# Performance work log

Measured on AMD Instinct MI355X. Metric: run time of the kernel, lower is better.

The kernel has to match this reference:

```python
import jax, jax.numpy as jnp
import numpy as np

N = 100000
E = 1600000
IN_C, HID, OUT_C = 500, 256, 40
K, ALPHA = 10, 0.1
LN_EPS = 1e-5


def setup_inputs() -> dict:
    key = jax.random.key(0)
    ks = jax.random.split(key, 12)
    glorot = lambda k, i, o: jax.random.normal(k, (i, o), jnp.float32) * (1.0 / np.sqrt(i))
    return {
        "x": jax.random.normal(ks[0], (N, IN_C), jnp.float32),
        "edge_index": jax.random.randint(ks[1], (2, E), 0, N, jnp.int64),
        "W1": glorot(ks[2], IN_C, HID), "b1": jnp.zeros((HID,), jnp.float32),
        "g1": jnp.ones((HID,), jnp.float32), "be1": jnp.zeros((HID,), jnp.float32),
        "W2": glorot(ks[3], HID, HID), "b2": jnp.zeros((HID,), jnp.float32),
        "g2": jnp.ones((HID,), jnp.float32), "be2": jnp.zeros((HID,), jnp.float32),
        "W3": glorot(ks[4], HID, OUT_C), "b3": jnp.zeros((OUT_C,), jnp.float32),
    }


def _layernorm(h, g, b):
    mu = jnp.mean(h, axis=-1, keepdims=True)
    var = jnp.mean(jnp.square(h - mu), axis=-1, keepdims=True)
    return (h - mu) * jax.lax.rsqrt(var + LN_EPS) * g + b


def reference(x, edge_index, W1, b1, g1, be1, W2, b2, g2, be2, W3, b3):
    # --- MLP (eval mode: dropout inactive) ---
    h = _layernorm(jax.nn.gelu(x @ W1 + b1, approximate=False), g1, be1)
    h = _layernorm(jax.nn.gelu(h @ W2 + b2, approximate=False), g2, be2)
    h = h @ W3 + b3  # [N, OUT_C]

    # --- GCN normalization with self-loops (PyG gcn_norm) ---
    loops = jnp.arange(N, dtype=edge_index.dtype)
    row = jnp.concatenate([edge_index[0], loops])  # source
    col = jnp.concatenate([edge_index[1], loops])  # target
    deg = jax.ops.segment_sum(jnp.ones_like(col, jnp.float32), col, num_segments=N)
    dinv = jnp.where(deg > 0, jax.lax.rsqrt(deg), 0.0)
    norm = dinv[row] * dinv[col]  # [E+N]

    # --- APPNP: K steps of h <- (1-alpha) * A_hat h + alpha * h0 ---
    h0 = h
    for _ in range(K):
        msg = norm[:, None] * h[row]                       # gather + scale
        agg = jax.ops.segment_sum(msg, col, num_segments=N)  # scatter-add
        h = (1.0 - ALPHA) * agg + ALPHA * h0
    return h
```

## Files before the change

### kernel.cpp

```cpp
#include <hip/hip_runtime.h>
#include <hip/hip_bf16.h>
#include <math.h>

#define N_NODES 100000
#define N_EDGES 1600000
#define IN_C    500
#define HID     256
#define OUT_C   40
#define K_ITERS 10
#define ALPHA   0.1f
#define LN_EPS  1e-5f

#define K1PAD   512
#define K2PAD   256

#define SCAN_CHUNK 1024
#define NBLK_SCAN  ((N_NODES + SCAN_CHUNK - 1) / SCAN_CHUNK)

typedef __attribute__((ext_vector_type(8))) short bf16x8;
typedef __attribute__((ext_vector_type(4))) float f32x4;

__device__ __forceinline__ void split2(float a, short& hi, short& lo) {
    const unsigned ua = __float_as_uint(a);
    hi = (short)(ua >> 16);
    const float r = a - __uint_as_float(ua & 0xffff0000u);
    lo = (short)(__float_as_uint(r) >> 16);
}

__device__ __forceinline__ void async_load16(const void* g, void* l) {
    __builtin_amdgcn_global_load_lds(
        (const __attribute__((address_space(1))) void*)g,
        (__attribute__((address_space(3))) void*)l, 16, 0, 0);
}

__global__ void deg_count_kernel(const int* __restrict__ col, int* __restrict__ cnt, int e) {
    int i = blockIdx.x * blockDim.x + threadIdx.x;
    if (i < e) atomicAdd(&cnt[col[i]], 1);
}

__global__ void dinv_kernel(const int* __restrict__ cnt, float* __restrict__ dinv, int n) {
    int i = blockIdx.x * blockDim.x + threadIdx.x;
    if (i < n) dinv[i] = rsqrtf((float)cnt[i] + 1.0f);
}

__global__ __launch_bounds__(256) void scan_partial_kernel(const int* __restrict__ cnt,
                                                           int* __restrict__ bsum) {
    __shared__ int s[256];
    const int base = blockIdx.x * SCAN_CHUNK;
    const int t = threadIdx.x;
    int sum = 0;
    #pragma unroll
    for (int j = 0; j < 4; j++) {
        int idx = base + t * 4 + j;
        if (idx < N_NODES) sum += cnt[idx];
    }
    s[t] = sum;
    __syncthreads();
    for (int off = 128; off > 0; off >>= 1) {
        if (t < off) s[t] += s[t + off];
        __syncthreads();
    }
    if (t == 0) bsum[blockIdx.x] = s[0];
}

__global__ __launch_bounds__(128) void scan_bsum_kernel(int* __restrict__ bsum, int nblk) {
    __shared__ int s[128];
    const int t = threadIdx.x;
    const int orig = (t < nblk) ? bsum[t] : 0;
    s[t] = orig;
    __syncthreads();
    for (int off = 1; off < 128; off <<= 1) {
        int v = 0;
        if (t >= off) v = s[t - off];
        __syncthreads();
        s[t] += v;
        __syncthreads();
    }
    if (t < nblk) bsum[t] = s[t] - orig;
}

__global__ __launch_bounds__(256) void scan_final_kernel(const int* __restrict__ cnt,
                                                         const int* __restrict__ bsum,
                                                         int* __restrict__ offs) {
    __shared__ int s[256];
    const int base = blockIdx.x * SCAN_CHUNK;
    const int t = threadIdx.x;
    int v[4];
    int lsum = 0;
    #pragma unroll
    for (int j = 0; j < 4; j++) {
        int idx = base + t * 4 + j;
        v[j] = (idx < N_NODES) ? cnt[idx] : 0;
        lsum += v[j];
    }
    s[t] = lsum;
    __syncthreads();
    const int orig = lsum;
    for (int off = 1; off < 256; off <<= 1) {
        int u = 0;
        if (t >= off) u = s[t - off];
        __syncthreads();
        s[t] += u;
        __syncthreads();
    }
    int run = bsum[blockIdx.x] + (s[t] - orig);
    #pragma unroll
    for (int j = 0; j < 4; j++) {
        int idx = base + t * 4 + j;
        if (idx < N_NODES) offs[idx] = run;
        run += v[j];
    }
}

__global__ void set_total_kernel(int* __restrict__ offs) {
    if (threadIdx.x == 0 && blockIdx.x == 0) offs[N_NODES] = N_EDGES;
}

__global__ void csr_fill_kernel(const int* __restrict__ row, const int* __restrict__ col,
                                const float* __restrict__ dinv, const int* __restrict__ offs,
                                int* __restrict__ cursor, int2* __restrict__ csr_ew, int e) {
    int i = blockIdx.x * blockDim.x + threadIdx.x;
    if (i >= e) return;
    const int r = row[i], c = col[i];
    const int p = offs[c] + atomicAdd(&cursor[c], 1);
    csr_ew[p] = make_int2(r, __float_as_int(dinv[r] * dinv[c]));
}

__global__ __launch_bounds__(256) void wsplit_kernel(
    const float* __restrict__ W, short* __restrict__ hi, short* __restrict__ lo,
    int K, int Nn, int Kpad)
{
    const int idx = blockIdx.x * 256 + threadIdx.x;
    if (idx >= Nn * Kpad) return;
    const int n = idx / Kpad, k = idx - n * Kpad;
    const float v = (k < K) ? W[(size_t)k * Nn + n] : 0.0f;
    short h, l;
    split2(v, h, l);
    hi[idx] = h;
    lo[idx] = l;
}

#define GBM 64
#define GBN 256
#define GBK 32

__global__ __launch_bounds__(256) void gemm1_fused_kernel(
    const float* __restrict__ X,
    const short* __restrict__ Bhi, const short* __restrict__ Blo,
    const float* __restrict__ bias, float* __restrict__ C, int M)
{
    __shared__ short As[2][GBM * GBK];
    __shared__ short Bs[2][GBN * GBK];

    const int tid  = threadIdx.x;
    const int wid  = tid >> 6, lane = tid & 63;
    const int wm   = wid >> 1, wn = wid & 1;
    const int fm   = lane & 15, fq = lane >> 4;
    const int row0 = blockIdx.x * GBM;

    const int ar   = tid >> 2;
    const int aseg = tid & 3;
    const int gr   = min(row0 + ar, M - 1);

    f32x4 acc[2][8] = {};

    for (int ks = 0; ks < K1PAD / GBK; ks++) {
        const int k0 = ks * GBK;
        __syncthreads();

        #pragma unroll
        for (int i = 0; i < 4; i++) {
            const int c  = i * 256 + tid;
            const int n  = c >> 2, k8 = (c & 3) * 8;
            const int cb = (i * 256 + wid * 64) * 8;
            const size_t oB = (size_t)n * K1PAD + k0 + k8;
            async_load16(Bhi + oB, &Bs[0][cb]);
            async_load16(Blo + oB, &Bs[1][cb]);
        }
        {
            const int kb = k0 + aseg * 8;
            float v[8];
            if (k0 + GBK <= IN_C) {
                const float4 v0 = *(const float4*)(X + (size_t)gr * IN_C + kb);
                const float4 v1 = *(const float4*)(X + (size_t)gr * IN_C + kb + 4);
                v[0]=v0.x; v[1]=v0.y; v[2]=v0.z; v[3]=v0.w;
                v[4]=v1.x; v[5]=v1.y; v[6]=v1.z; v[7]=v1.w;
            } else {
                #pragma unroll
                for (int j = 0; j < 8; j++)
                    v[j] = (kb + j < IN_C) ? X[(size_t)gr * IN_C + kb + j] : 0.0f;
            }
            bf16x8 h8, l8;
            #pragma unroll
            for (int j = 0; j < 8; j++) { short th, tl; split2(v[j], th, tl); h8[j] = th; l8[j] = tl; }
            *(bf16x8*)&As[0][ar * GBK + aseg * 8] = h8;
            *(bf16x8*)&As[1][ar * GBK + aseg * 8] = l8;
        }
        __syncthreads();

        bf16x8 ah[2], al[2];
        #pragma unroll
        for (int tm = 0; tm < 2; tm++) {
            const int r = wm * 32 + tm * 16 + fm;
            ah[tm] = *(const bf16x8*)&As[0][r * GBK + fq * 8];
            al[tm] = *(const bf16x8*)&As[1][r * GBK + fq * 8];
        }
        #pragma unroll
        for (int tn = 0; tn < 8; tn++) {
            const int cc = wn * 128 + tn * 16 + fm;
            const bf16x8 bh = *(const bf16x8*)&Bs[0][cc * GBK + fq * 8];
            const bf16x8 bl = *(const bf16x8*)&Bs[1][cc * GBK + fq * 8];
            #pragma unroll
            for (int tm = 0; tm < 2; tm++) {
                acc[tm][tn] = __builtin_amdgcn_mfma_f32_16x16x32_bf16(ah[tm], bh, acc[tm][tn], 0, 0, 0);
                acc[tm][tn] = __builtin_amdgcn_mfma_f32_16x16x32_bf16(ah[tm], bl, acc[tm][tn], 0, 0, 0);
                acc[tm][tn] = __builtin_amdgcn_mfma_f32_16x16x32_bf16(al[tm], bh, acc[tm][tn], 0, 0, 0);
            }
        }
    }

    #pragma unroll
    for (int tm = 0; tm < 2; tm++) {
        #pragma unroll
        for (int tn = 0; tn < 8; tn++) {
            const int gc = wn * 128 + tn * 16 + fm;
            const float bv = bias[gc];
            #pragma unroll
            for (int r = 0; r < 4; r++) {
                const int gr2 = row0 + wm * 32 + tm * 16 + fq * 4 + r;
                if (gr2 < M) {
                    float v = acc[tm][tn][r] + bv;
                    v = 0.5f * v * (1.0f + erff(v * 0.70710678118654752f));
                    C[(size_t)gr2 * 256 + gc] = v;
                }
            }
        }
    }
}

__global__ __launch_bounds__(256) void gemm2_kernel(
    const short* __restrict__ Ahi, const short* __restrict__ Alo,
    const short* __restrict__ Bhi, const short* __restrict__ Blo,
    const float* __restrict__ bias, float* __restrict__ C, int M)
{
    __shared__ short As[2][GBM * GBK];
    __shared__ short Bs[2][GBN * GBK];

    const int tid  = threadIdx.x;
    const int wid  = tid >> 6, lane = tid & 63;
    const int wm   = wid >> 1, wn = wid & 1;
    const int fm   = lane & 15, fq = lane >> 4;
    const int row0 = blockIdx.x * GBM;

    f32x4 acc[2][8] = {};

    for (int ks = 0; ks < K2PAD / GBK; ks++) {
        const int k0 = ks * GBK;
        __syncthreads();

        #pragma unroll
        for (int i = 0; i < 4; i++) {
            const int c  = i * 256 + tid;
            const int n  = c >> 2, k8 = (c & 3) * 8;
            const int cb = (i * 256 + wid * 64) * 8;
            const size_t oB = (size_t)n * K2PAD + k0 + k8;
            async_load16(Bhi + oB, &Bs[0][cb]);
            async_load16(Blo + oB, &Bs[1][cb]);
        }
        {
            const int m  = tid >> 2, k8 = (tid & 3) * 8;
            const int cb = (wid * 64) * 8;
            const size_t oA = (size_t)min(row0 + m, M - 1) * K2PAD + k0 + k8;
            async_load16(Ahi + oA, &As[0][cb]);
            async_load16(Alo + oA, &As[1][cb]);
        }
        __syncthreads();

        bf16x8 ah[2], al[2];
        #pragma unroll
        for (int tm = 0; tm < 2; tm++) {
            const int r = wm * 32 + tm * 16 + fm;
            ah[tm] = *(const bf16x8*)&As[0][r * GBK + fq * 8];
            al[tm] = *(const bf16x8*)&As[1][r * GBK + fq * 8];
        }
        #pragma unroll
        for (int tn = 0; tn < 8; tn++) {
            const int cc = wn * 128 + tn * 16 + fm;
            const bf16x8 bh = *(const bf16x8*)&Bs[0][cc * GBK + fq * 8];
            const bf16x8 bl = *(const bf16x8*)&Bs[1][cc * GBK + fq * 8];
            #pragma unroll
            for (int tm = 0; tm < 2; tm++) {
                acc[tm][tn] = __builtin_amdgcn_mfma_f32_16x16x32_bf16(ah[tm], bh, acc[tm][tn], 0, 0, 0);
                acc[tm][tn] = __builtin_amdgcn_mfma_f32_16x16x32_bf16(ah[tm], bl, acc[tm][tn], 0, 0, 0);
                acc[tm][tn] = __builtin_amdgcn_mfma_f32_16x16x32_bf16(al[tm], bh, acc[tm][tn], 0, 0, 0);
            }
        }
    }

    #pragma unroll
    for (int tm = 0; tm < 2; tm++) {
        #pragma unroll
        for (int tn = 0; tn < 8; tn++) {
            const int gc = wn * 128 + tn * 16 + fm;
            const float bv = bias[gc];
            #pragma unroll
            for (int r = 0; r < 4; r++) {
                const int gr2 = row0 + wm * 32 + tm * 16 + fq * 4 + r;
                if (gr2 < M) {
                    float v = acc[tm][tn][r] + bv;
                    v = 0.5f * v * (1.0f + erff(v * 0.70710678118654752f));
                    C[(size_t)gr2 * 256 + gc] = v;
                }
            }
        }
    }
}

__global__ __launch_bounds__(256) void layernorm_split_kernel(
    const float* __restrict__ h, const float* __restrict__ g, const float* __restrict__ b,
    short* __restrict__ hi, short* __restrict__ lo, int nrows)
{
    const int wave = threadIdx.x >> 6;
    const int lane = threadIdx.x & 63;
    const int row  = blockIdx.x * 4 + wave;
    if (row >= nrows) return;

    const float* p = h + (size_t)row * HID;
    float v[4];
    float s = 0.0f;
    #pragma unroll
    for (int j = 0; j < 4; j++) { v[j] = p[lane + 64 * j]; s += v[j]; }
    #pragma unroll
    for (int off = 32; off > 0; off >>= 1) s += __shfl_xor(s, off);
    const float mu = s * (1.0f / 256.0f);

    float vs = 0.0f;
    #pragma unroll
    for (int j = 0; j < 4; j++) { float d = v[j] - mu; vs += d * d; }
    #pragma unroll
    for (int off = 32; off > 0; off >>= 1) vs += __shfl_xor(vs, off);
    const float rs = rsqrtf(vs * (1.0f / 256.0f) + LN_EPS);

    #pragma unroll
    for (int j = 0; j < 4; j++) {
        const int c = lane + 64 * j;
        const float o = (v[j] - mu) * rs * g[c] + b[c];
        short th, tl;
        split2(o, th, tl);
        hi[(size_t)row * HID + c] = th;
        lo[(size_t)row * HID + c] = tl;
    }
}

__global__ __launch_bounds__(256) void layernorm_kernel(
    float* __restrict__ h, const float* __restrict__ g, const float* __restrict__ b, int nrows)
{
    const int wave = threadIdx.x >> 6;
    const int lane = threadIdx.x & 63;
    const int row  = blockIdx.x * 4 + wave;
    if (row >= nrows) return;

    float* p = h + (size_t)row * HID;
    float v[4];
    float s = 0.0f;
    #pragma unroll
    for (int j = 0; j < 4; j++) { v[j] = p[lane + 64 * j]; s += v[j]; }
    #pragma unroll
    for (int off = 32; off > 0; off >>= 1) s += __shfl_xor(s, off);
    const float mu = s * (1.0f / 256.0f);

    float vs = 0.0f;
    #pragma unroll
    for (int j = 0; j < 4; j++) { float d = v[j] - mu; vs += d * d; }
    #pragma unroll
    for (int off = 32; off > 0; off >>= 1) vs += __shfl_xor(vs, off);
    const float rs = rsqrtf(vs * (1.0f / 256.0f) + LN_EPS);

    #pragma unroll
    for (int j = 0; j < 4; j++) {
        int c = lane + 64 * j;
        p[c] = (v[j] - mu) * rs * g[c] + b[c];
    }
}

__global__ __launch_bounds__(256) void gemm3_kernel(
    const float* __restrict__ A, const float* __restrict__ W,
    const float* __restrict__ bias, float* __restrict__ C, int M)
{
    __shared__ float Ws[HID * OUT_C];
    __shared__ float bs[OUT_C];
    for (int i = threadIdx.x; i < HID * OUT_C; i += 256) Ws[i] = W[i];
    if (threadIdx.x < OUT_C) bs[threadIdx.x] = bias[threadIdx.x];
    __syncthreads();

    const int total = M * OUT_C;
    for (int idx = blockIdx.x * 256 + threadIdx.x; idx < total; idx += gridDim.x * 256) {
        const int r = idx / OUT_C;
        const int c = idx - r * OUT_C;
        const float4* a4 = reinterpret_cast<const float4*>(A + (size_t)r * HID);
        float s = 0.0f;
        #pragma unroll 4
        for (int k4 = 0; k4 < HID / 4; k4++) {
            float4 av = a4[k4];
            const float* wp = &Ws[k4 * 4 * OUT_C + c];
            s += av.x * wp[0] + av.y * wp[OUT_C] + av.z * wp[2 * OUT_C] + av.w * wp[3 * OUT_C];
        }
        C[idx] = s + bs[c];
    }
}

__global__ __launch_bounds__(256) void appnp_kernel(
    const int* __restrict__ offs, const int2* __restrict__ csr_ew,
    const float* __restrict__ dinv,
    const float* __restrict__ h, const float* __restrict__ h0,
    float* __restrict__ out)
{
    const int node = blockIdx.x * 4 + (threadIdx.x >> 6);
    if (node >= N_NODES) return;
    const int lane = threadIdx.x & 63;
    const int g = lane / 10;
    const int q = lane - g * 10;
    const bool act = (lane < 60);

    const int start = offs[node];
    const int end   = offs[node + 1];

    float ax = 0.0f, ay = 0.0f, az = 0.0f, aw = 0.0f;
    for (int e0 = start; e0 < end; e0 += 6) {
        const int  ee = e0 + g;
        const bool ea = act && (ee < end);
        const int2 ed = csr_ew[ea ? ee : start];
        const float w = ea ? __int_as_float(ed.y) : 0.0f;
        const float4 hv = *(const float4*)(h + (size_t)ed.x * OUT_C + q * 4);
        ax += w * hv.x; ay += w * hv.y; az += w * hv.z; aw += w * hv.w;
    }

    ax += __shfl(ax, lane + 30); ay += __shfl(ay, lane + 30);
    az += __shfl(az, lane + 30); aw += __shfl(aw, lane + 30);
    {
        const float bx = __shfl(ax, lane + 10), cx = __shfl(ax, lane + 20);
        const float by = __shfl(ay, lane + 10), cy = __shfl(ay, lane + 20);
        const float bz = __shfl(az, lane + 10), cz = __shfl(az, lane + 20);
        const float bw = __shfl(aw, lane + 10), cw = __shfl(aw, lane + 20);
        ax += bx + cx; ay += by + cy; az += bz + cz; aw += bw + cw;
    }

    if (lane < 10) {
        const float d = dinv[node];
        const float self = d * d;
        const size_t idx = (size_t)node * OUT_C + lane * 4;
        const float4 hs  = *(const float4*)(h + idx);
        const float4 h0v = *(const float4*)(h0 + idx);
        float4 o;
        o.x = (1.0f - ALPHA) * (ax + self * hs.x) + ALPHA * h0v.x;
        o.y = (1.0f - ALPHA) * (ay + self * hs.y) + ALPHA * h0v.y;
        o.z = (1.0f - ALPHA) * (az + self * hs.z) + ALPHA * h0v.z;
        o.w = (1.0f - ALPHA) * (aw + self * hs.w) + ALPHA * h0v.w;
        *(float4*)(out + idx) = o;
    }
}

extern "C" void kernel_launch(void* const* d_in, const int* in_sizes, int n_in,
                              void* d_out, int out_size, void* d_ws, size_t ws_size,
                              hipStream_t stream) {
    const float* x   = (const float*)d_in[0];
    const int*   ei  = (const int*)d_in[1];
    const float* W1  = (const float*)d_in[2];
    const float* b1  = (const float*)d_in[3];
    const float* g1  = (const float*)d_in[4];
    const float* be1 = (const float*)d_in[5];
    const float* W2  = (const float*)d_in[6];
    const float* b2  = (const float*)d_in[7];
    const float* g2  = (const float*)d_in[8];
    const float* be2 = (const float*)d_in[9];
    const float* W3  = (const float*)d_in[10];
    const float* b3  = (const float*)d_in[11];
    float* out = (float*)d_out;

    const int* e_row = ei;
    const int* e_col = ei + N_EDGES;

    float* ws = (float*)d_ws;
    size_t off = 0;
    float* dinv = ws + off; off += N_NODES;
    int*   cnt  = (int*)(ws + off); off += N_NODES;
    int*   offs = (int*)(ws + off); off += N_NODES + 1;
    int*   bsum = (int*)(ws + off); off += 128 + 3;
    short* W1hi = (short*)(ws + off); off += 65536;
    short* W1lo = (short*)(ws + off); off += 65536;
    short* W2hi = (short*)(ws + off); off += 32768;
    short* W2lo = (short*)(ws + off); off += 32768;
    float* t1 = ws + off; off += (size_t)N_NODES * HID;
    float* t2 = t1;
    float* regA = ws + off; off += (size_t)N_NODES * HID;
    short* A2hi = (short*)regA;
    short* A2lo = A2hi + (size_t)N_NODES * HID;
    int2*  csr_ew = (int2*)regA;
    float* h0 = regA + 2 * (size_t)N_EDGES;
    float* hA = h0 + (size_t)N_NODES * OUT_C;
    float* hB = hA + (size_t)N_NODES * OUT_C;

    hipMemsetAsync(cnt, 0, N_NODES * sizeof(int), stream);
    deg_count_kernel<<<(N_EDGES + 255) / 256, 256, 0, stream>>>(e_col, cnt, N_EDGES);
    dinv_kernel<<<(N_NODES + 255) / 256, 256, 0, stream>>>(cnt, dinv, N_NODES);
    scan_partial_kernel<<<NBLK_SCAN, 256, 0, stream>>>(cnt, bsum);
    scan_bsum_kernel<<<1, 128, 0, stream>>>(bsum, NBLK_SCAN);
    scan_final_kernel<<<NBLK_SCAN, 256, 0, stream>>>(cnt, bsum, offs);
    set_total_kernel<<<1, 64, 0, stream>>>(offs);

    wsplit_kernel<<<(256 * K1PAD + 255) / 256, 256, 0, stream>>>(W1, W1hi, W1lo, IN_C, 256, K1PAD);
    wsplit_kernel<<<(256 * K2PAD + 255) / 256, 256, 0, stream>>>(W2, W2hi, W2lo, HID, 256, K2PAD);

    {
        const int nblk = (N_NODES + GBM - 1) / GBM;
        gemm1_fused_kernel<<<nblk, 256, 0, stream>>>(x, W1hi, W1lo, b1, t1, N_NODES);
        layernorm_split_kernel<<<(N_NODES + 3) / 4, 256, 0, stream>>>(t1, g1, be1, A2hi, A2lo, N_NODES);
        gemm2_kernel<<<nblk, 256, 0, stream>>>(A2hi, A2lo, W2hi, W2lo, b2, t2, N_NODES);
        layernorm_kernel<<<(N_NODES + 3) / 4, 256, 0, stream>>>(t2, g2, be2, N_NODES);
        gemm3_kernel<<<2048, 256, 0, stream>>>(t2, W3, b3, h0, N_NODES);
    }

    hipMemsetAsync(cnt, 0, N_NODES * sizeof(int), stream);
    csr_fill_kernel<<<(N_EDGES + 255) / 256, 256, 0, stream>>>(
        e_row, e_col, dinv, offs, cnt, csr_ew, N_EDGES);

    const float* hcur = h0;
    for (int it = 0; it < K_ITERS; it++) {
        float* tgt = (it == K_ITERS - 1) ? out : ((it & 1) ? hB : hA);
        appnp_kernel<<<(N_NODES + 3) / 4, 256, 0, stream>>>(
            offs, csr_ew, dinv, hcur, h0, tgt);
        hcur = tgt;
    }
}
```

Measured before the change: 1.579 ms.

## Double GEMM row tile and map six nodes per wave in APPNP propagation

GEMM1 and GEMM2 now use a 128-row block tile, so each wave handles four 16-row MMA tiles and each B tile loaded from global memory feeds twice as many rows. The APPNP kernel now gives each 10-lane group its own node, so one wave processes six nodes and loops over their edges two at a time. This removes the cross-lane shuffle reduction and the per-edge lane waste seen with roughly 17 edges per node. The risks are higher accumulator register pressure in the GEMMs, which can lower occupancy, and load imbalance between the six nodes that share a wave.

New measurement: 1.761 ms. +11.5%, slower.

```diff
diff --git a/kernel.cpp b/kernel.cpp
--- a/kernel.cpp
+++ b/kernel.cpp
@@ -140,7 +140,7 @@
     lo[idx] = l;
 }
 
-#define GBM 64
+#define GBM 128
 #define GBN 256
 #define GBK 32
 
@@ -158,11 +158,11 @@
     const int fm   = lane & 15, fq = lane >> 4;
     const int row0 = blockIdx.x * GBM;
 
-    const int ar   = tid >> 2;
-    const int aseg = tid & 3;
+    const int ar   = tid >> 1;
+    const int aseg = tid & 1;
     const int gr   = min(row0 + ar, M - 1);
 
-    f32x4 acc[2][8] = {};
+    f32x4 acc[4][8] = {};
 
     for (int ks = 0; ks < K1PAD / GBK; ks++) {
         const int k0 = ks * GBK;
@@ -178,30 +178,37 @@
             async_load16(Blo + oB, &Bs[1][cb]);
         }
         {
-            const int kb = k0 + aseg * 8;
-            float v[8];
-            if (k0 + GBK <= IN_C) {
-                const float4 v0 = *(const float4*)(X + (size_t)gr * IN_C + kb);
-                const float4 v1 = *(const float4*)(X + (size_t)gr * IN_C + kb + 4);
-                v[0]=v0.x; v[1]=v0.y; v[2]=v0.z; v[3]=v0.w;
-                v[4]=v1.x; v[5]=v1.y; v[6]=v1.z; v[7]=v1.w;
+            const int kb = k0 + aseg * 16;
+            float v[16];
+            if (kb + 16 <= IN_C) {
+                #pragma unroll
+                for (int i = 0; i < 4; i++) {
+                    const float4 t4 = *(const float4*)(X + (size_t)gr * IN_C + kb + i * 4);
+                    v[i*4+0] = t4.x; v[i*4+1] = t4.y; v[i*4+2] = t4.z; v[i*4+3] = t4.w;
+                }
             } else {
                 #pragma unroll
-                for (int j = 0; j < 8; j++)
+                for (int j = 0; j < 16; j++)
                     v[j] = (kb + j < IN_C) ? X[(size_t)gr * IN_C + kb + j] : 0.0f;
             }
-            bf16x8 h8, l8;
+            bf16x8 h0, h1, l0, l1;
             #pragma unroll
-            for (int j = 0; j < 8; j++) { short th, tl; split2(v[j], th, tl); h8[j] = th; l8[j] = tl; }
-            *(bf16x8*)&As[0][ar * GBK + aseg * 8] = h8;
-            *(bf16x8*)&As[1][ar * GBK + aseg * 8] = l8;
-        }
-        __syncthreads();
-
-        bf16x8 ah[2], al[2];
-        #pragma unroll
-        for (int tm = 0; tm < 2; tm++) {
-            const int r = wm * 32 + tm * 16 + fm;
+            for (int j = 0; j < 8; j++) {
+                short th, tl;
+                split2(v[j], th, tl);     h0[j] = th; l0[j] = tl;
+                split2(v[j + 8], th, tl); h1[j] = th; l1[j] = tl;
+            }
+            *(bf16x8*)&As[0][ar * GBK + aseg * 16]     = h0;
+            *(bf16x8*)&As[0][ar * GBK + aseg * 16 + 8] = h1;
+            *(bf16x8*)&As[1][ar * GBK + aseg * 16]     = l0;
+            *(bf16x8*)&As[1][ar * GBK + aseg * 16 + 8] = l1;
+        }
+        __syncthreads();
+
+        bf16x8 ah[4], al[4];
+        #pragma unroll
+        for (int tm = 0; tm < 4; tm++) {
+            const int r = wm * 64 + tm * 16 + fm;
             ah[tm] = *(const bf16x8*)&As[0][r * GBK + fq * 8];
             al[tm] = *(const bf16x8*)&As[1][r * GBK + fq * 8];
         }
@@ -211,7 +218,7 @@
             const bf16x8 bh = *(const bf16x8*)&Bs[0][cc * GBK + fq * 8];
             const bf16x8 bl = *(const bf16x8*)&Bs[1][cc * GBK + fq * 8];
             #pragma unroll
-            for (int tm = 0; tm < 2; tm++) {
+            for (int tm = 0; tm < 4; tm++) {
                 acc[tm][tn] = __builtin_amdgcn_mfma_f32_16x16x32_bf16(ah[tm], bh, acc[tm][tn], 0, 0, 0);
                 acc[tm][tn] = __builtin_amdgcn_mfma_f32_16x16x32_bf16(ah[tm], bl, acc[tm][tn], 0, 0, 0);
                 acc[tm][tn] = __builtin_amdgcn_mfma_f32_16x16x32_bf16(al[tm], bh, acc[tm][tn], 0, 0, 0);
@@ -220,14 +227,14 @@
     }
 
     #pragma unroll
-    for (int tm = 0; tm < 2; tm++) {
+    for (int tm = 0; tm < 4; tm++) {
         #pragma unroll
         for (int tn = 0; tn < 8; tn++) {
             const int gc = wn * 128 + tn * 16 + fm;
             const float bv = bias[gc];
             #pragma unroll
             for (int r = 0; r < 4; r++) {
-                const int gr2 = row0 + wm * 32 + tm * 16 + fq * 4 + r;
+                const int gr2 = row0 + wm * 64 + tm * 16 + fq * 4 + r;
                 if (gr2 < M) {
                     float v = acc[tm][tn][r] + bv;
                     v = 0.5f * v * (1.0f + erff(v * 0.70710678118654752f));
@@ -252,7 +259,7 @@
     const int fm   = lane & 15, fq = lane >> 4;
     const int row0 = blockIdx.x * GBM;
 
-    f32x4 acc[2][8] = {};
+    f32x4 acc[4][8] = {};
 
     for (int ks = 0; ks < K2PAD / GBK; ks++) {
         const int k0 = ks * GBK;
@@ -267,19 +274,21 @@
             async_load16(Bhi + oB, &Bs[0][cb]);
             async_load16(Blo + oB, &Bs[1][cb]);
         }
-        {
-            const int m  = tid >> 2, k8 = (tid & 3) * 8;
-            const int cb = (wid * 64) * 8;
+        #pragma unroll
+        for (int i = 0; i < 2; i++) {
+            const int c  = i * 256 + tid;
+            const int m  = c >> 2, k8 = (c & 3) * 8;
+            const int cb = (i * 256 + wid * 64) * 8;
             const size_t oA = (size_t)min(row0 + m, M - 1) * K2PAD + k0 + k8;
             async_load16(Ahi + oA, &As[0][cb]);
             async_load16(Alo + oA, &As[1][cb]);
         }
         __syncthreads();
 
-        bf16x8 ah[2], al[2];
-        #pragma unroll
-        for (int tm = 0; tm < 2; tm++) {
-            const int r = wm * 32 + tm * 16 + fm;
+        bf16x8 ah[4], al[4];
+        #pragma unroll
+        for (int tm = 0; tm < 4; tm++) {
+            const int r = wm * 64 + tm * 16 + fm;
             ah[tm] = *(const bf16x8*)&As[0][r * GBK + fq * 8];
             al[tm] = *(const bf16x8*)&As[1][r * GBK + fq * 8];
         }
@@ -289,7 +298,7 @@
             const bf16x8 bh = *(const bf16x8*)&Bs[0][cc * GBK + fq * 8];
             const bf16x8 bl = *(const bf16x8*)&Bs[1][cc * GBK + fq * 8];
             #pragma unroll
-            for (int tm = 0; tm < 2; tm++) {
+            for (int tm = 0; tm < 4; tm++) {
                 acc[tm][tn] = __builtin_amdgcn_mfma_f32_16x16x32_bf16(ah[tm], bh, acc[tm][tn], 0, 0, 0);
                 acc[tm][tn] = __builtin_amdgcn_mfma_f32_16x16x32_bf16(ah[tm], bl, acc[tm][tn], 0, 0, 0);
                 acc[tm][tn] = __builtin_amdgcn_mfma_f32_16x16x32_bf16(al[tm], bh, acc[tm][tn], 0, 0, 0);
@@ -298,14 +307,14 @@
     }
 
     #pragma unroll
-    for (int tm = 0; tm < 2; tm++) {
+    for (int tm = 0; tm < 4; tm++) {
         #pragma unroll
         for (int tn = 0; tn < 8; tn++) {
             const int gc = wn * 128 + tn * 16 + fm;
             const float bv = bias[gc];
             #pragma unroll
             for (int r = 0; r < 4; r++) {
-                const int gr2 = row0 + wm * 32 + tm * 16 + fq * 4 + r;
+                const int gr2 = row0 + wm * 64 + tm * 16 + fq * 4 + r;
                 if (gr2 < M) {
                     float v = acc[tm][tn][r] + bv;
                     v = 0.5f * v * (1.0f + erff(v * 0.70710678118654752f));
@@ -415,40 +424,41 @@
     const float* __restrict__ h, const float* __restrict__ h0,
     float* __restrict__ out)
 {
-    const int node = blockIdx.x * 4 + (threadIdx.x >> 6);
-    if (node >= N_NODES) return;
+    const int wv   = blockIdx.x * 4 + (threadIdx.x >> 6);
     const int lane = threadIdx.x & 63;
-    const int g = lane / 10;
-    const int q = lane - g * 10;
-    const bool act = (lane < 60);
-
-    const int start = offs[node];
-    const int end   = offs[node + 1];
+    const int s    = lane / 10;
+    const int q    = lane - s * 10;
+    const int node = wv * 6 + s;
+    const bool act = (s < 6) && (node < N_NODES);
+
+    int start = 0, end = 0;
+    if (act) { start = offs[node]; end = offs[node + 1]; }
 
     float ax = 0.0f, ay = 0.0f, az = 0.0f, aw = 0.0f;
-    for (int e0 = start; e0 < end; e0 += 6) {
-        const int  ee = e0 + g;
-        const bool ea = act && (ee < end);
-        const int2 ed = csr_ew[ea ? ee : start];
-        const float w = ea ? __int_as_float(ed.y) : 0.0f;
-        const float4 hv = *(const float4*)(h + (size_t)ed.x * OUT_C + q * 4);
-        ax += w * hv.x; ay += w * hv.y; az += w * hv.z; aw += w * hv.w;
-    }
-
-    ax += __shfl(ax, lane + 30); ay += __shfl(ay, lane + 30);
-    az += __shfl(az, lane + 30); aw += __shfl(aw, lane + 30);
-    {
-        const float bx = __shfl(ax, lane + 10), cx = __shfl(ax, lane + 20);
-        const float by = __shfl(ay, lane + 10), cy = __shfl(ay, lane + 20);
-        const float bz = __shfl(az, lane + 10), cz = __shfl(az, lane + 20);
-        const float bw = __shfl(aw, lane + 10), cw = __shfl(aw, lane + 20);
-        ax += bx + cx; ay += by + cy; az += bz + cz; aw += bw + cw;
-    }
-
-    if (lane < 10) {
+    int e = start;
+    for (; e + 2 <= end; e += 2) {
+        const int2 d0 = csr_ew[e];
+        const int2 d1 = csr_ew[e + 1];
+        const float w0 = __int_as_float(d0.y);
+        const float w1 = __int_as_float(d1.y);
+        const float4 v0 = *(const float4*)(h + (size_t)d0.x * OUT_C + q * 4);
+        const float4 v1 = *(const float4*)(h + (size_t)d1.x * OUT_C + q * 4);
+        ax += w0 * v0.x + w1 * v1.x;
+        ay += w0 * v0.y + w1 * v1.y;
+        az += w0 * v0.z + w1 * v1.z;
+        aw += w0 * v0.w + w1 * v1.w;
+    }
+    if (e < end) {
+        const int2 d0 = csr_ew[e];
+        const float w0 = __int_as_float(d0.y);
+        const float4 v0 = *(const float4*)(h + (size_t)d0.x * OUT_C + q * 4);
+        ax += w0 * v0.x; ay += w0 * v0.y; az += w0 * v0.z; aw += w0 * v0.w;
+    }
+
+    if (act) {
         const float d = dinv[node];
         const float self = d * d;
-        const size_t idx = (size_t)node * OUT_C + lane * 4;
+        const size_t idx = (size_t)node * OUT_C + q * 4;
         const float4 hs  = *(const float4*)(h + idx);
         const float4 h0v = *(const float4*)(h0 + idx);
         float4 o;
@@ -524,11 +534,12 @@
     csr_fill_kernel<<<(N_EDGES + 255) / 256, 256, 0, stream>>>(
         e_row, e_col, dinv, offs, cnt, csr_ew, N_EDGES);
 
+    const int nwaves = (N_NODES + 5) / 6;
+    const int ablk   = (nwaves + 3) / 4;
     const float* hcur = h0;
     for (int it = 0; it < K_ITERS; it++) {
         float* tgt = (it == K_ITERS - 1) ? out : ((it & 1) ? hB : hA);
-        appnp_kernel<<<(N_NODES + 3) / 4, 256, 0, stream>>>(
-            offs, csr_ew, dinv, hcur, h0, tgt);
+        appnp_kernel<<<ablk, 256, 0, stream>>>(offs, csr_ew, dinv, hcur, h0, tgt);
         hcur = tgt;
     }
 }
```

## Split APPNP features into 8-channel planes and propagate chunk by chunk

Applied to the files above, without the earlier changes.

The MLP output h0 and the propagation buffers are stored as five planes of 8 channels each instead of row-major 40-channel rows. Each APPNP iteration then launches one kernel per plane. In that kernel every node is handled by two lanes, each walking its edge list with a 2-way unrolled gather, instead of one wavefront per node. The aim is to shrink the gathered working set per pass to about 3.2 MB so it stays in L2, and to remove the cross-lane shuffle reduction. In exchange the CSR is re-read five times per iteration, there are five times as many launches, and lanes within a wavefront diverge when node degrees differ.

After: 2.138 ms. +35.4%, slower.

```diff
diff --git a/kernel.cpp b/kernel.cpp
--- a/kernel.cpp
+++ b/kernel.cpp
@@ -13,6 +13,9 @@
 
 #define K1PAD   512
 #define K2PAD   256
+
+#define N_CHUNK 5
+#define CH_PER  8
 
 #define SCAN_CHUNK 1024
 #define NBLK_SCAN  ((N_NODES + SCAN_CHUNK - 1) / SCAN_CHUNK)
@@ -385,7 +388,7 @@
 
 __global__ __launch_bounds__(256) void gemm3_kernel(
     const float* __restrict__ A, const float* __restrict__ W,
-    const float* __restrict__ bias, float* __restrict__ C, int M)
+    const float* __restrict__ bias, float* __restrict__ Cc, int M)
 {
     __shared__ float Ws[HID * OUT_C];
     __shared__ float bs[OUT_C];
@@ -405,58 +408,58 @@
             const float* wp = &Ws[k4 * 4 * OUT_C + c];
             s += av.x * wp[0] + av.y * wp[OUT_C] + av.z * wp[2 * OUT_C] + av.w * wp[3 * OUT_C];
         }
-        C[idx] = s + bs[c];
-    }
-}
-
-__global__ __launch_bounds__(256) void appnp_kernel(
+        Cc[(size_t)(c >> 3) * M * CH_PER + (size_t)r * CH_PER + (c & 7)] = s + bs[c];
+    }
+}
+
+__global__ __launch_bounds__(256) void appnp_chunk_kernel(
     const int* __restrict__ offs, const int2* __restrict__ csr_ew,
     const float* __restrict__ dinv,
-    const float* __restrict__ h, const float* __restrict__ h0,
-    float* __restrict__ out)
-{
-    const int node = blockIdx.x * 4 + (threadIdx.x >> 6);
-    if (node >= N_NODES) return;
+    const float* __restrict__ h_c, const float* __restrict__ h0_c,
+    float* __restrict__ tgt, int rs)
+{
     const int lane = threadIdx.x & 63;
-    const int g = lane / 10;
-    const int q = lane - g * 10;
-    const bool act = (lane < 60);
-
-    const int start = offs[node];
-    const int end   = offs[node + 1];
-
-    float ax = 0.0f, ay = 0.0f, az = 0.0f, aw = 0.0f;
-    for (int e0 = start; e0 < end; e0 += 6) {
-        const int  ee = e0 + g;
-        const bool ea = act && (ee < end);
-        const int2 ed = csr_ew[ea ? ee : start];
-        const float w = ea ? __int_as_float(ed.y) : 0.0f;
-        const float4 hv = *(const float4*)(h + (size_t)ed.x * OUT_C + q * 4);
-        ax += w * hv.x; ay += w * hv.y; az += w * hv.z; aw += w * hv.w;
-    }
-
-    ax += __shfl(ax, lane + 30); ay += __shfl(ay, lane + 30);
-    az += __shfl(az, lane + 30); aw += __shfl(aw, lane + 30);
-    {
-        const float bx = __shfl(ax, lane + 10), cx = __shfl(ax, lane + 20);
-        const float by = __shfl(ay, lane + 10), cy = __shfl(ay, lane + 20);
-        const float bz = __shfl(az, lane + 10), cz = __shfl(az, lane + 20);
-        const float bw = __shfl(aw, lane + 10), cw = __shfl(aw, lane + 20);
-        ax += bx + cx; ay += by + cy; az += bz + cz; aw += bw + cw;
-    }
-
-    if (lane < 10) {
+    const int s    = lane >> 1;
+    const int hf   = lane & 1;
+    const int node = (blockIdx.x * 4 + (threadIdx.x >> 6)) * 32 + s;
+    const bool act = (node < N_NODES);
+
+    int start = 0, end = 0;
+    if (act) { start = offs[node]; end = offs[node + 1]; }
+
+    float4 a = make_float4(0.0f, 0.0f, 0.0f, 0.0f);
+    int e = start;
+    for (; e + 2 <= end; e += 2) {
+        const int2 d0 = csr_ew[e];
+        const int2 d1 = csr_ew[e + 1];
+        const float w0 = __int_as_float(d0.y);
+        const float w1 = __int_as_float(d1.y);
+        const float4 v0 = *(const float4*)(h_c + (size_t)d0.x * CH_PER + hf * 4);
+        const float4 v1 = *(const float4*)(h_c + (size_t)d1.x * CH_PER + hf * 4);
+        a.x += w0 * v0.x + w1 * v1.x;
+        a.y += w0 * v0.y + w1 * v1.y;
+        a.z += w0 * v0.z + w1 * v1.z;
+        a.w += w0 * v0.w + w1 * v1.w;
+    }
+    if (e < end) {
+        const int2 d0 = csr_ew[e];
+        const float w0 = __int_as_float(d0.y);
+        const float4 v0 = *(const float4*)(h_c + (size_t)d0.x * CH_PER + hf * 4);
+        a.x += w0 * v0.x; a.y += w0 * v0.y; a.z += w0 * v0.z; a.w += w0 * v0.w;
+    }
+
+    if (act) {
         const float d = dinv[node];
         const float self = d * d;
-        const size_t idx = (size_t)node * OUT_C + lane * 4;
-        const float4 hs  = *(const float4*)(h + idx);
-        const float4 h0v = *(const float4*)(h0 + idx);
+        const size_t ic = (size_t)node * CH_PER + hf * 4;
+        const float4 hs  = *(const float4*)(h_c + ic);
+        const float4 h0v = *(const float4*)(h0_c + ic);
         float4 o;
-        o.x = (1.0f - ALPHA) * (ax + self * hs.x) + ALPHA * h0v.x;
-        o.y = (1.0f - ALPHA) * (ay + self * hs.y) + ALPHA * h0v.y;
-        o.z = (1.0f - ALPHA) * (az + self * hs.z) + ALPHA * h0v.z;
-        o.w = (1.0f - ALPHA) * (aw + self * hs.w) + ALPHA * h0v.w;
-        *(float4*)(out + idx) = o;
+        o.x = (1.0f - ALPHA) * (a.x + self * hs.x) + ALPHA * h0v.x;
+        o.y = (1.0f - ALPHA) * (a.y + self * hs.y) + ALPHA * h0v.y;
+        o.z = (1.0f - ALPHA) * (a.z + self * hs.z) + ALPHA * h0v.z;
+        o.w = (1.0f - ALPHA) * (a.w + self * hs.w) + ALPHA * h0v.w;
+        *(float4*)(tgt + (size_t)node * rs + hf * 4) = o;
     }
 }
 
@@ -524,11 +527,21 @@
     csr_fill_kernel<<<(N_EDGES + 255) / 256, 256, 0, stream>>>(
         e_row, e_col, dinv, offs, cnt, csr_ew, N_EDGES);
 
+    const int ablk = (N_NODES + 127) / 128;
     const float* hcur = h0;
+    float* hnxt = hA;
     for (int it = 0; it < K_ITERS; it++) {
-        float* tgt = (it == K_ITERS - 1) ? out : ((it & 1) ? hB : hA);
-        appnp_kernel<<<(N_NODES + 3) / 4, 256, 0, stream>>>(
-            offs, csr_ew, dinv, hcur, h0, tgt);
-        hcur = tgt;
-    }
-}
+        for (int c = 0; c < N_CHUNK; c++) {
+            const size_t plane = (size_t)c * N_NODES * CH_PER;
+            float* tgt; int rs;
+            if (it == K_ITERS - 1) { tgt = out + c * CH_PER; rs = OUT_C; }
+            else                   { tgt = hnxt + plane;     rs = CH_PER; }
+            appnp_chunk_kernel<<<ablk, 256, 0, stream>>>(
+                offs, csr_ew, dinv, hcur + plane, h0 + plane, tgt, rs);
+        }
+        const float* t = hcur;
+        hcur = hnxt;
+        hnxt = (it == 0) ? hB : (float*)t;
+        if (it == 0) hnxt = hB;
+    }
+}
```
